# Optimization experiments

Hardware: AMD Instinct MI355X
Metric: run time of the kernel (lower is better)

The kernel has to match this reference:

```python
import jax, jax.numpy as jnp
import numpy as np

NNODES = 128
BS = 1024
MAX_ST = (NNODES + 1) ** 2   # 16641
MAX_ST1 = NNODES ** 2        # 16384
AT_LEN = NNODES + 1          # 129
MAXOUT = AT_LEN + MAX_ST + MAX_ST1  # 33154
HIDDEN = 512
OUT_DIM = AT_LEN             # 129


def setup_inputs() -> dict:
    key = jax.random.key(0)
    ks = jax.random.split(key, 6)
    st = jax.random.normal(ks[0], (BS, MAX_ST), dtype=jnp.float32)
    at = jax.random.normal(ks[1], (BS, AT_LEN), dtype=jnp.float32)
    st1 = jax.random.normal(ks[2], (BS, MAX_ST1), dtype=jnp.float32)
    # MLP params (self.layers): Linear(MAXOUT->HIDDEN) + ReLU + Linear(HIDDEN->OUT_DIM)
    W1 = jax.random.normal(ks[3], (MAXOUT, HIDDEN), dtype=jnp.float32) * (1.0 / np.sqrt(MAXOUT))
    b1 = jnp.zeros((HIDDEN,), dtype=jnp.float32)
    W2 = jax.random.normal(ks[4], (HIDDEN, OUT_DIM), dtype=jnp.float32) * (1.0 / np.sqrt(HIDDEN))
    b2 = jnp.zeros((OUT_DIM,), dtype=jnp.float32)
    return {"st": st, "at": at, "st1": st1, "W1": W1, "b1": b1, "W2": W2, "b2": b2}


def reference(st, at, st1, W1, b1, W2, b2):
    # Batched equivalent of the per-sample Python loop:
    # per sample: cat(pad(st.flatten(), maxSt), at, pad(st1.flatten(), maxSt1)) -> layers -> cat outputs.
    # st/st1 are already at padded sizes here, so concat directly along features.
    x = jnp.concatenate([st, at, st1], axis=1)          # [B, MAXOUT]
    h = jax.nn.relu(x @ W1 + b1)                        # [B, HIDDEN]
    out = h @ W2 + b2                                   # [B, OUT_DIM]
    return out.reshape(-1)                              # concatenated 1-D outputs, matching torch.cat
```

## Files before the change

kernel.cpp:

```cpp
#include <hip/hip_runtime.h>

#define BATCH 1024
#define STSZ 16641
#define ATSZ 129
#define ST1SZ 16384
#define K1 33154
#define K1P 33280
#define HID 512
#define ODIM 129
#define NKT 520
#define NSLICE 32
#define NPACKX (33 * 1024)
#define NPACKW (NKT * 8)

typedef __bf16 bf16;
typedef bf16 bf16x8 __attribute__((ext_vector_type(8)));
typedef float floatx4 __attribute__((ext_vector_type(4)));
typedef float f32x4u __attribute__((ext_vector_type(4), aligned(4)));

typedef __attribute__((address_space(3))) unsigned int as3_uint;
typedef __attribute__((address_space(1))) unsigned int as1_uint;

__device__ __forceinline__ unsigned short f2bf(float f) {
  unsigned int u = __float_as_uint(f);
  unsigned int r = (u + 0x7FFFu + ((u >> 16) & 1u)) >> 16;
  return (unsigned short)r;
}
__device__ __forceinline__ float bf2f(unsigned short s) {
  unsigned int u = ((unsigned int)s) << 16;
  return __uint_as_float(u);
}

__device__ __forceinline__ void gload_lds16(const unsigned short* g, unsigned short* l) {
  __builtin_amdgcn_global_load_lds((const as1_uint*)g, (as3_uint*)l, 16, 0, 0);
}

__global__ __launch_bounds__(256) void packAll(const float* __restrict__ st,
                                               const float* __restrict__ at,
                                               const float* __restrict__ st1,
                                               const float* __restrict__ W1,
                                               unsigned short* __restrict__ Xb,
                                               unsigned short* __restrict__ W1t) {
  __shared__ unsigned short tile[64][72];
  int bb  = blockIdx.x;
  int tid = threadIdx.x;

  if (bb < NPACKX) {
    int bx = bb % 33;
    int b  = bb / 33;
    int g  = bx * 256 + tid;
    if (g >= K1P / 4) return;
    int col = g * 4;
    const float* srow  = st  + (long)b * STSZ;
    const float* arow  = at  + (long)b * ATSZ;
    const float* s1row = st1 + (long)b * ST1SZ;

    float4 v;
    if (col + 3 < STSZ) {
      f32x4u t = *(const f32x4u*)(srow + col);
      v = make_float4(t.x, t.y, t.z, t.w);
    } else if (col >= STSZ + ATSZ && col + 3 < K1) {
      f32x4u t = *(const f32x4u*)(s1row + (col - (STSZ + ATSZ)));
      v = make_float4(t.x, t.y, t.z, t.w);
    } else if (col >= STSZ && col + 3 < STSZ + ATSZ) {
      f32x4u t = *(const f32x4u*)(arow + (col - STSZ));
      v = make_float4(t.x, t.y, t.z, t.w);
    } else if (col >= K1) {
      v = make_float4(0.f, 0.f, 0.f, 0.f);
    } else {
      float e[4];
#pragma unroll
      for (int j = 0; j < 4; ++j) {
        int p = col + j;
        if (p < STSZ)                 e[j] = srow[p];
        else if (p < STSZ + ATSZ)     e[j] = arow[p - STSZ];
        else if (p < K1)              e[j] = s1row[p - (STSZ + ATSZ)];
        else                          e[j] = 0.f;
      }
      v = make_float4(e[0], e[1], e[2], e[3]);
    }
    unsigned short o[4] = { f2bf(v.x), f2bf(v.y), f2bf(v.z), f2bf(v.w) };
    *(ushort4*)&Xb[(long)b * K1P + col] = *(const ushort4*)o;
  } else {
    int lb = bb - NPACKX;
    int k0 = (lb % NKT) * 64;
    int n0 = (lb / NKT) * 64;
    int nt = (tid & 15) * 4;
    int kr = tid >> 4;
#pragma unroll
    for (int p = 0; p < 4; ++p) {
      int k = p * 16 + kr;
      int kk = k0 + k;
      float4 v = make_float4(0.f, 0.f, 0.f, 0.f);
      if (kk < K1) v = *(const float4*)&W1[(long)kk * HID + n0 + nt];
      unsigned short o[4] = { f2bf(v.x), f2bf(v.y), f2bf(v.z), f2bf(v.w) };
      *(ushort4*)&tile[k][nt] = *(const ushort4*)o;
    }
    __syncthreads();
    int kt = (tid & 15) * 4;
    int nr = tid >> 4;
#pragma unroll
    for (int p = 0; p < 4; ++p) {
      int n = p * 16 + nr;
      unsigned short o[4] = { tile[kt][n], tile[kt + 1][n], tile[kt + 2][n], tile[kt + 3][n] };
      *(ushort4*)&W1t[(long)(n0 + n) * K1P + k0 + kt] = *(const ushort4*)o;
    }
  }
}

__global__ __launch_bounds__(256, 4) void gemm1(const unsigned short* __restrict__ Xb,
                                                const unsigned short* __restrict__ W1t,
                                                unsigned short* __restrict__ part) {
  __shared__ __align__(16) unsigned short lA[128 * 64];
  __shared__ __align__(16) unsigned short lB[128 * 64];

  int hB  = blockIdx.x;
  int xcd = hB & 7;
  int idx = hB >> 3;
  int gidx = xcd * 32 + (idx >> 2);
  int nt = idx & 3;
  int mt = gidx & 7;
  int s  = gidx >> 3;
  int t0 = s * 16 + (s < 8 ? s : 8);
  int tc = 16 + (s < 8 ? 1 : 0);

  int tid = threadIdx.x;
  int wave = tid >> 6;
  int lane = tid & 63;
  int wm = (wave & 1) * 64;
  int wn = (wave >> 1) * 64;

  floatx4 acc[4][4] = {};

  const unsigned short* Ab = Xb  + (long)(mt * 128) * K1P;
  const unsigned short* Bb = W1t + (long)(nt * 128) * K1P;

  int srow = lane >> 3;
  int scol = ((lane & 7) ^ srow) * 8;

  int sr = lane & 7;

  for (int it = 0; it < tc; ++it) {
    long kOff = (long)(t0 + it) * 64;
#pragma unroll
    for (int r = 0; r < 4; ++r) {
      int c = wave * 4 + r;
      int row = c * 8 + srow;
      gload_lds16(Ab + (long)row * K1P + kOff + scol, &lA[c * 512 + lane * 8]);
      gload_lds16(Bb + (long)row * K1P + kOff + scol, &lB[c * 512 + lane * 8]);
    }
    __syncthreads();
#pragma unroll
    for (int ks = 0; ks < 2; ++ks) {
      int q = ks * 4 + (lane >> 4);
      int kidx = ((q ^ sr)) * 8;
      bf16x8 af[4], bfr[4];
#pragma unroll
      for (int i = 0; i < 4; ++i)
        af[i] = *(const bf16x8*)&lA[(wm + i * 16 + (lane & 15)) * 64 + kidx];
#pragma unroll
      for (int j = 0; j < 4; ++j)
        bfr[j] = *(const bf16x8*)&lB[(wn + j * 16 + (lane & 15)) * 64 + kidx];
#pragma unroll
      for (int i = 0; i < 4; ++i)
#pragma unroll
        for (int j = 0; j < 4; ++j)
          acc[i][j] = __builtin_amdgcn_mfma_f32_16x16x32_bf16(af[i], bfr[j], acc[i][j], 0, 0, 0);
    }
    __syncthreads();
  }

  unsigned short* P = part + (long)s * BATCH * HID;
  int cn = nt * 128 + wn + (lane & 15);
  int rbase = mt * 128 + wm + (lane >> 4) * 4;
#pragma unroll
  for (int i = 0; i < 4; ++i)
#pragma unroll
    for (int j = 0; j < 4; ++j)
#pragma unroll
      for (int r = 0; r < 4; ++r)
        P[(long)(rbase + i * 16 + r) * HID + cn + j * 16] = f2bf(acc[i][j][r]);
}

__global__ __launch_bounds__(256) void reduceGemm2(const unsigned short* __restrict__ part,
                                                   const float* __restrict__ b1,
                                                   const float* __restrict__ W2,
                                                   const float* __restrict__ b2,
                                                   float* __restrict__ out) {
  __shared__ float hs[HID];
  int m = blockIdx.x;
  int t = threadIdx.x;

  float2 bv = ((const float2*)b1)[t];
  float a0 = bv.x, a1 = bv.y;
#pragma unroll
  for (int s = 0; s < NSLICE; ++s) {
    unsigned int u = *(const unsigned int*)&part[((long)s * BATCH + m) * HID + 2 * t];
    a0 += bf2f((unsigned short)(u & 0xffffu));
    a1 += bf2f((unsigned short)(u >> 16));
  }
  hs[2 * t]     = fmaxf(a0, 0.f);
  hs[2 * t + 1] = fmaxf(a1, 0.f);
  __syncthreads();

  if (t < ODIM) {
    float c0 = 0.f, c1 = 0.f, c2 = 0.f, c3 = 0.f;
#pragma unroll 4
    for (int k = 0; k < HID; k += 4) {
      c0 += hs[k]     * W2[(long)(k)     * ODIM + t];
      c1 += hs[k + 1] * W2[(long)(k + 1) * ODIM + t];
      c2 += hs[k + 2] * W2[(long)(k + 2) * ODIM + t];
      c3 += hs[k + 3] * W2[(long)(k + 3) * ODIM + t];
    }
    out[(long)m * ODIM + t] = ((c0 + c1) + (c2 + c3)) + b2[t];
  }
}

extern "C" void kernel_launch(void* const* d_in, const int* in_sizes, int n_in,
                              void* d_out, int out_size, void* d_ws, size_t ws_size,
                              hipStream_t stream) {
  const float* st  = (const float*)d_in[0];
  const float* at  = (const float*)d_in[1];
  const float* st1 = (const float*)d_in[2];
  const float* W1  = (const float*)d_in[3];
  const float* b1  = (const float*)d_in[4];
  const float* W2  = (const float*)d_in[5];
  const float* b2  = (const float*)d_in[6];
  float* out = (float*)d_out;

  char* ws = (char*)d_ws;
  unsigned short* Xb   = (unsigned short*)ws;
  unsigned short* W1t  = (unsigned short*)(ws + (size_t)BATCH * K1P * 2);
  unsigned short* part = (unsigned short*)(ws + (size_t)BATCH * K1P * 2 + (size_t)HID * K1P * 2);

  packAll<<<dim3(NPACKX + NPACKW), 256, 0, stream>>>(st, at, st1, W1, Xb, W1t);
  gemm1<<<dim3(1024), 256, 0, stream>>>(Xb, W1t, part);
  reduceGemm2<<<dim3(BATCH), 256, 0, stream>>>(part, b1, W2, b2, out);
}
```

Baseline: 299.4 us.

## Coarsen pack and reduce kernels per row, relax gemm1 occupancy bound

The X-pack path now uses one block per batch row looping over 33 column chunks instead of one block per chunk. The reduce/GEMM2 kernel handles four rows per block so each W2 element is loaded once and reused across four rows. gemm1's launch bound drops from 4 to 3 blocks per CU, leaving more registers per thread, and the W1 transpose tile padding changes from 72 to 68. Together these aim to cut launch/block overhead and W2 traffic, at the cost of fewer blocks and less parallelism in the pack and reduce stages.

```diff
diff --git a/kernel.cpp b/kernel.cpp
--- a/kernel.cpp
+++ b/kernel.cpp
@@ -10,7 +10,6 @@
 #define ODIM 129
 #define NKT 520
 #define NSLICE 32
-#define NPACKX (33 * 1024)
 #define NPACKW (NKT * 8)
 
 typedef __bf16 bf16;
@@ -41,48 +40,50 @@
                                                const float* __restrict__ W1,
                                                unsigned short* __restrict__ Xb,
                                                unsigned short* __restrict__ W1t) {
-  __shared__ unsigned short tile[64][72];
+  __shared__ unsigned short tile[64][68];
   int bb  = blockIdx.x;
   int tid = threadIdx.x;
 
-  if (bb < NPACKX) {
-    int bx = bb % 33;
-    int b  = bb / 33;
-    int g  = bx * 256 + tid;
-    if (g >= K1P / 4) return;
-    int col = g * 4;
+  if (bb < BATCH) {
+    int b = bb;
     const float* srow  = st  + (long)b * STSZ;
     const float* arow  = at  + (long)b * ATSZ;
     const float* s1row = st1 + (long)b * ST1SZ;
-
-    float4 v;
-    if (col + 3 < STSZ) {
-      f32x4u t = *(const f32x4u*)(srow + col);
-      v = make_float4(t.x, t.y, t.z, t.w);
-    } else if (col >= STSZ + ATSZ && col + 3 < K1) {
-      f32x4u t = *(const f32x4u*)(s1row + (col - (STSZ + ATSZ)));
-      v = make_float4(t.x, t.y, t.z, t.w);
-    } else if (col >= STSZ && col + 3 < STSZ + ATSZ) {
-      f32x4u t = *(const f32x4u*)(arow + (col - STSZ));
-      v = make_float4(t.x, t.y, t.z, t.w);
-    } else if (col >= K1) {
-      v = make_float4(0.f, 0.f, 0.f, 0.f);
-    } else {
-      float e[4];
-#pragma unroll
-      for (int j = 0; j < 4; ++j) {
-        int p = col + j;
-        if (p < STSZ)                 e[j] = srow[p];
-        else if (p < STSZ + ATSZ)     e[j] = arow[p - STSZ];
-        else if (p < K1)              e[j] = s1row[p - (STSZ + ATSZ)];
-        else                          e[j] = 0.f;
+#pragma unroll 2
+    for (int i = 0; i < 33; ++i) {
+      int g = i * 256 + tid;
+      if (g < K1P / 4) {
+        int col = g * 4;
+        float4 v;
+        if (col + 3 < STSZ) {
+          f32x4u t = *(const f32x4u*)(srow + col);
+          v = make_float4(t.x, t.y, t.z, t.w);
+        } else if (col >= STSZ + ATSZ && col + 3 < K1) {
+          f32x4u t = *(const f32x4u*)(s1row + (col - (STSZ + ATSZ)));
+          v = make_float4(t.x, t.y, t.z, t.w);
+        } else if (col >= STSZ && col + 3 < STSZ + ATSZ) {
+          f32x4u t = *(const f32x4u*)(arow + (col - STSZ));
+          v = make_float4(t.x, t.y, t.z, t.w);
+        } else if (col >= K1) {
+          v = make_float4(0.f, 0.f, 0.f, 0.f);
+        } else {
+          float e[4];
+#pragma unroll
+          for (int j = 0; j < 4; ++j) {
+            int p = col + j;
+            if (p < STSZ)                 e[j] = srow[p];
+            else if (p < STSZ + ATSZ)     e[j] = arow[p - STSZ];
+            else if (p < K1)              e[j] = s1row[p - (STSZ + ATSZ)];
+            else                          e[j] = 0.f;
+          }
+          v = make_float4(e[0], e[1], e[2], e[3]);
+        }
+        unsigned short o[4] = { f2bf(v.x), f2bf(v.y), f2bf(v.z), f2bf(v.w) };
+        *(ushort4*)&Xb[(long)b * K1P + col] = *(const ushort4*)o;
       }
-      v = make_float4(e[0], e[1], e[2], e[3]);
-    }
-    unsigned short o[4] = { f2bf(v.x), f2bf(v.y), f2bf(v.z), f2bf(v.w) };
-    *(ushort4*)&Xb[(long)b * K1P + col] = *(const ushort4*)o;
+    }
   } else {
-    int lb = bb - NPACKX;
+    int lb = bb - BATCH;
     int k0 = (lb % NKT) * 64;
     int n0 = (lb / NKT) * 64;
     int nt = (tid & 15) * 4;
@@ -108,7 +109,7 @@
   }
 }
 
-__global__ __launch_bounds__(256, 4) void gemm1(const unsigned short* __restrict__ Xb,
+__global__ __launch_bounds__(256, 3) void gemm1(const unsigned short* __restrict__ Xb,
                                                 const unsigned short* __restrict__ W1t,
                                                 unsigned short* __restrict__ part) {
   __shared__ __align__(16) unsigned short lA[128 * 64];
@@ -187,32 +188,40 @@
                                                    const float* __restrict__ W2,
                                                    const float* __restrict__ b2,
                                                    float* __restrict__ out) {
-  __shared__ float hs[HID];
-  int m = blockIdx.x;
+  __shared__ float hs[4][HID];
+  int m0 = blockIdx.x * 4;
   int t = threadIdx.x;
 
   float2 bv = ((const float2*)b1)[t];
-  float a0 = bv.x, a1 = bv.y;
-#pragma unroll
-  for (int s = 0; s < NSLICE; ++s) {
-    unsigned int u = *(const unsigned int*)&part[((long)s * BATCH + m) * HID + 2 * t];
-    a0 += bf2f((unsigned short)(u & 0xffffu));
-    a1 += bf2f((unsigned short)(u >> 16));
-  }
-  hs[2 * t]     = fmaxf(a0, 0.f);
-  hs[2 * t + 1] = fmaxf(a1, 0.f);
+#pragma unroll
+  for (int r = 0; r < 4; ++r) {
+    float a0 = bv.x, a1 = bv.y;
+#pragma unroll
+    for (int s = 0; s < NSLICE; ++s) {
+      unsigned int u = *(const unsigned int*)&part[((long)s * BATCH + m0 + r) * HID + 2 * t];
+      a0 += bf2f((unsigned short)(u & 0xffffu));
+      a1 += bf2f((unsigned short)(u >> 16));
+    }
+    hs[r][2 * t]     = fmaxf(a0, 0.f);
+    hs[r][2 * t + 1] = fmaxf(a1, 0.f);
+  }
   __syncthreads();
 
   if (t < ODIM) {
     float c0 = 0.f, c1 = 0.f, c2 = 0.f, c3 = 0.f;
 #pragma unroll 4
-    for (int k = 0; k < HID; k += 4) {
-      c0 += hs[k]     * W2[(long)(k)     * ODIM + t];
-      c1 += hs[k + 1] * W2[(long)(k + 1) * ODIM + t];
-      c2 += hs[k + 2] * W2[(long)(k + 2) * ODIM + t];
-      c3 += hs[k + 3] * W2[(long)(k + 3) * ODIM + t];
-    }
-    out[(long)m * ODIM + t] = ((c0 + c1) + (c2 + c3)) + b2[t];
+    for (int k = 0; k < HID; ++k) {
+      float w = W2[(long)k * ODIM + t];
+      c0 += hs[0][k] * w;
+      c1 += hs[1][k] * w;
+      c2 += hs[2][k] * w;
+      c3 += hs[3][k] * w;
+    }
+    float bt = b2[t];
+    out[(long)(m0 + 0) * ODIM + t] = c0 + bt;
+    out[(long)(m0 + 1) * ODIM + t] = c1 + bt;
+    out[(long)(m0 + 2) * ODIM + t] = c2 + bt;
+    out[(long)(m0 + 3) * ODIM + t] = c3 + bt;
   }
 }
 
@@ -233,7 +242,7 @@
   unsigned short* W1t  = (unsigned short*)(ws + (size_t)BATCH * K1P * 2);
   unsigned short* part = (unsigned short*)(ws + (size_t)BATCH * K1P * 2 + (size_t)HID * K1P * 2);
 
-  packAll<<<dim3(NPACKX + NPACKW), 256, 0, stream>>>(st, at, st1, W1, Xb, W1t);
+  packAll<<<dim3(BATCH + NPACKW), 256, 0, stream>>>(st, at, st1, W1, Xb, W1t);
   gemm1<<<dim3(1024), 256, 0, stream>>>(Xb, W1t, part);
-  reduceGemm2<<<dim3(BATCH), 256, 0, stream>>>(part, b1, W2, b2, out);
-}
+  reduceGemm2<<<dim3(BATCH / 4), 256, 0, stream>>>(part, b1, W2, b2, out);
+}
```

Result: slower. 347.2 us (+16.0%).
